# Kernel optimization log

Measured on AMD Instinct MI355X. Metric: run time of the kernel, lower is better.

The kernel has to match this reference:

```python
import jax, jax.numpy as jnp
import numpy as np

N_NODES = 50000
N_EDGES = 1000000
F = 256          # feature_size
NC = 300         # n_content_dims
ED = 64          # embedding_dim = 2**int(log2(F/4))
L = 3            # n_layers


def setup_inputs() -> dict:
    key = jax.random.key(0)
    ks = jax.random.split(key, 20)
    s = 0.05  # weight init scale
    return {
        'node_ids': jnp.arange(N_NODES, dtype=jnp.int32),
        'content': jax.random.normal(ks[0], (N_NODES, NC), jnp.float32),
        'src': jax.random.randint(ks[1], (N_EDGES,), 0, N_NODES, jnp.int32),
        'dst': jax.random.randint(ks[2], (N_EDGES,), 0, N_NODES, jnp.int32),
        'emb': jax.random.normal(ks[3], (N_NODES + 1, ED), jnp.float32) / ED,
        'W_exp': jax.random.normal(ks[4], (F, ED), jnp.float32) * s,
        'b_exp': jnp.zeros((F,), jnp.float32),
        'W_p1': jax.random.normal(ks[5], (NC, NC), jnp.float32) * s,
        'b_p1': jnp.zeros((NC,), jnp.float32),
        'W_p2': jax.random.normal(ks[6], (F, NC), jnp.float32) * s,
        'b_p2': jnp.zeros((F,), jnp.float32),
        'W_conv': jax.random.normal(ks[7], (L, F, 2 * F), jnp.float32) * s,
        'b_conv': jnp.zeros((L, F), jnp.float32),
        'Wo1': jax.random.normal(ks[8], (L - 1, F, F), jnp.float32) * s,
        'bo1': jnp.zeros((L - 1, F), jnp.float32),
        'Wo2': jax.random.normal(ks[9], (L - 1, F, F), jnp.float32) * s,
        'bo2': jnp.zeros((L - 1, F), jnp.float32),
    }


def _lrelu(x):
    return jax.nn.leaky_relu(x, 0.1)


def reference(node_ids, content, src, dst, emb, W_exp, b_exp, W_p1, b_p1,
              W_p2, b_p2, W_conv, b_conv, Wo1, bo1, Wo2, bo2):
    # initial node repr: expansion(node_emb) + proj(content)  (GaussianNoise = identity at eval)
    h = _lrelu(emb[node_ids] @ W_exp.T + b_exp)                 # [N, F]
    c = _lrelu(content @ W_p1.T + b_p1)
    c = _lrelu(c @ W_p2.T + b_p2)
    h = h + c

    ones = jnp.ones((src.shape[0],), h.dtype)
    deg = jax.ops.segment_sum(ones, dst, num_segments=N_NODES)  # in-degree
    w = (deg + 1.0)[:, None]                                    # +1 for self-loop

    for i in range(L):
        # message passing: sum neighbor h (with self-loop), then neighbor mean
        agg = jax.ops.segment_sum(h[src], dst, num_segments=N_NODES) + h  # [N, F]
        h_agg = (agg - h) / jnp.maximum(w - 1.0, 1.0)
        h_concat = jnp.concatenate([h, h_agg], axis=1)          # [N, 2F]
        h_new = h_concat @ W_conv[i].T + b_conv[i]
        if i < L - 1:
            h_new = _lrelu(h_new)
        # L2-normalize rows
        h_new = h_new / jnp.maximum(
            jnp.linalg.norm(h_new, axis=1, keepdims=True), 1e-6)
        if i < L - 1:  # W_out block (non-prediction layers)
            h_new = _lrelu(h_new @ Wo1[i].T + bo1[i])
            h_new = h_new @ Wo2[i].T + bo2[i]
        h = h_new
    return h
```

## Files before the change

kernel.cpp:

```cpp
#include <hip/hip_runtime.h>
#include <stdint.h>

#define NNODES 50000
#define NROWS_PAD 50048
#define NEDGES 1000000
#define FD 256
#define NCPAD 384
#define EDIM 64
#define NSCAN ((NNODES + 255) / 256)

typedef unsigned short u16;
typedef __attribute__((ext_vector_type(8))) short short8;
typedef __attribute__((ext_vector_type(4))) float floatx4;

__device__ __forceinline__ float bf2f(u16 x) {
    union { unsigned u; float f; } c; c.u = ((unsigned)x) << 16; return c.f;
}
__device__ __forceinline__ u16 f2bf(float f) {
    union { float f; unsigned u; } c; c.f = f;
    unsigned u = c.u;
    return (u16)((u + 0x7fffu + ((u >> 16) & 1u)) >> 16);
}
__device__ __forceinline__ void gload16(const u16* g, u16* l) {
    __builtin_amdgcn_global_load_lds(
        (const __attribute__((address_space(1))) void*)g,
        (__attribute__((address_space(3))) void*)l, 16, 0, 0);
}

__global__ void detect_kernel(const u16* p, int* flag) {
    __shared__ int smax;
    if (threadIdx.x == 0) smax = 0;
    __syncthreads();
    int m = 0;
    for (int i = threadIdx.x; i < 8192; i += 256) {
        int e = (p[i] >> 7) & 0xFF;
        m = m > e ? m : e;
    }
    atomicMax(&smax, m);
    __syncthreads();
    if (threadIdx.x == 0) *flag = (smax >= 140) ? 1 : 0;
}

#define NB_CONV 1798
#define NB_CNT4 489
#define PREP_GRID (NB_CONV + NB_CNT4)
__global__ __launch_bounds__(512) void prep_kernel(
    u16* arena, const int* flagp,
    const void* wexp, const void* bexp, const void* wp1, const void* bp1,
    const void* wp2, const void* bp2, const void* wconv, const void* bconv,
    const void* wo1, const void* bo1, const void* wo2, const void* bo2,
    const int* dst, int* deg)
{
    const int bid = blockIdx.x;
    if (bid >= NB_CONV) {
        int q4 = (bid - NB_CONV) * 512 + threadIdx.x;
        if (q4 * 4 + 3 < NEDGES) {
            int4 d = *(const int4*)(dst + q4 * 4);
            atomicAdd(&deg[d.x], 1);
            atomicAdd(&deg[d.y], 1);
            atomicAdd(&deg[d.z], 1);
            atomicAdd(&deg[d.w], 1);
        }
        return;
    }
    const int offs[13]  = {0,16384,16640,164096,164480,262784,263040,
                           656256,657024,788096,788608,919680,920192};
    const int rreal[12] = {256,1,300,1,256,1,768,1,512,1,512,1};
    const int creal[12] = {64,256,300,300,300,256,512,768,256,512,256,512};
    const int cpd[12]   = {64,256,384,384,384,256,512,768,256,512,256,512};
    long gid = (long)bid * 512 + threadIdx.x;
    if (gid >= 920192) return;
    const void* srcs[12] = {wexp,bexp,wp1,bp1,wp2,bp2,wconv,bconv,wo1,bo1,wo2,bo2};
    int fl = *flagp;
    int t = 0;
    #pragma unroll
    for (int i = 1; i < 12; ++i) if (gid >= offs[i]) t = i;
    long local = gid - offs[t];
    int rr = (int)(local / cpd[t]);
    int cc = (int)(local % cpd[t]);
    u16 v = 0;
    if (rr < rreal[t] && cc < creal[t]) {
        long si = (long)rr * creal[t] + cc;
        v = fl ? f2bf(((const float*)srcs[t])[si]) : ((const u16*)srcs[t])[si];
    }
    arena[gid] = v;
}

__global__ __launch_bounds__(256) void scan1_kernel(const int* deg, int* bsum) {
    __shared__ int s[256];
    int t = threadIdx.x;
    int i = blockIdx.x * 256 + t;
    s[t] = (i < NNODES) ? deg[i] : 0;
    __syncthreads();
    #pragma unroll
    for (int off = 128; off > 0; off >>= 1) {
        if (t < off) s[t] += s[t + off];
        __syncthreads();
    }
    if (t == 0) bsum[blockIdx.x] = s[0];
}

__global__ __launch_bounds__(256) void scan2_kernel(int* bsum, int* row_start) {
    __shared__ int s[256];
    int t = threadIdx.x;
    int v = (t < NSCAN) ? bsum[t] : 0;
    s[t] = v;
    __syncthreads();
    for (int off = 1; off < 256; off <<= 1) {
        int x = (t >= off) ? s[t - off] : 0;
        __syncthreads();
        s[t] += x;
        __syncthreads();
    }
    if (t < NSCAN) bsum[t] = s[t] - v;
    if (t == 0) row_start[NNODES] = NEDGES;
}

__global__ __launch_bounds__(256) void scan3_kernel(const int* deg, const int* bsum,
        int* row_start, int* cursor, float* inv_w) {
    __shared__ int s[256];
    int t = threadIdx.x;
    int i = blockIdx.x * 256 + t;
    int v = (i < NNODES) ? deg[i] : 0;
    s[t] = v;
    __syncthreads();
    for (int off = 1; off < 256; off <<= 1) {
        int x = (t >= off) ? s[t - off] : 0;
        __syncthreads();
        s[t] += x;
        __syncthreads();
    }
    if (i < NNODES) {
        int base = bsum[blockIdx.x] + s[t] - v;
        row_start[i] = base;
        cursor[i] = base;
        inv_w[i] = 1.0f / (float)(v > 0 ? v : 1);
    }
}

#define IF_GRID (391 * 7)
__global__ __launch_bounds__(512, 4) void initfill_kernel(
    const void* __restrict__ content, const void* __restrict__ emb,
    const int* __restrict__ flagp,
    const u16* __restrict__ Wp1, const u16* __restrict__ bp1,
    const u16* __restrict__ Wp2, const u16* __restrict__ bp2,
    const u16* __restrict__ Wexp, const u16* __restrict__ bexp,
    u16* __restrict__ hbuf,
    const int* __restrict__ src, const int* __restrict__ dst,
    int* __restrict__ cursor, int* __restrict__ esrc)
{
    __shared__ __align__(16) u16 sA[64 * 64];
    __shared__ __align__(16) u16 sB[384 * 32];
    __shared__ __align__(16) u16 T[64 * 384];

    const int g7 = blockIdx.x / 7, r7 = blockIdx.x % 7;
    if (r7 >= 2) {
        int fb = g7 * 5 + (r7 - 2);
        int e = fb * 512 + threadIdx.x;
        if (e < NEDGES) {
            int v = dst[e];
            int pos = atomicAdd(&cursor[v], 1);
            if ((unsigned)pos < (unsigned)NEDGES) esrc[pos] = src[e];
        }
        return;
    }
    const int bm = (g7 * 2 + r7) * 64;
    const int t = threadIdx.x;
    const int wave = t >> 6, lane = t & 63;
    const int quad = lane >> 4, l16 = lane & 15;
    const int wm = wave >> 2, wn = wave & 3;
    const int lrow = lane >> 2, lcol = (lane & 3) * 8;
    const int fl = *flagp;

    {
        int row = t >> 3;
        int c0 = (t & 7) * 8;
        int gm = bm + row;
        u16 o[8];
        if (gm < NNODES) {
            if (fl) {
                const float* ep = (const float*)emb + (size_t)gm * EDIM + c0;
                float4 x = *(const float4*)ep;
                float4 y = *(const float4*)(ep + 4);
                o[0]=f2bf(x.x); o[1]=f2bf(x.y); o[2]=f2bf(x.z); o[3]=f2bf(x.w);
                o[4]=f2bf(y.x); o[5]=f2bf(y.y); o[6]=f2bf(y.z); o[7]=f2bf(y.w);
            } else {
                const u16* ep = (const u16*)emb + (size_t)gm * EDIM + c0;
                ushort4 x = *(const ushort4*)ep;
                ushort4 y = *(const ushort4*)(ep + 4);
                o[0]=x.x; o[1]=x.y; o[2]=x.z; o[3]=x.w;
                o[4]=y.x; o[5]=y.y; o[6]=y.z; o[7]=y.w;
            }
        } else {
            #pragma unroll
            for (int k = 0; k < 8; ++k) o[k] = 0;
        }
        u16* d = &sA[(row * 64 + c0) ^ ((row & 7) << 3)];
        #pragma unroll
        for (int k = 0; k < 8; ++k) d[k] = o[k];
    }
    #pragma unroll
    for (int j = 0; j < 6; ++j) {
        int idx = (j * 512 + t) * 8;
        int row = idx / 384;
        int c0 = idx % 384;
        int gm = bm + row;
        u16 o[8];
        if (gm < NNODES && c0 + 8 <= 300) {
            if (fl) {
                const float* cp = (const float*)content + (size_t)gm * 300 + c0;
                float4 x = *(const float4*)cp;
                float4 y = *(const float4*)(cp + 4);
                o[0]=f2bf(x.x); o[1]=f2bf(x.y); o[2]=f2bf(x.z); o[3]=f2bf(x.w);
                o[4]=f2bf(y.x); o[5]=f2bf(y.y); o[6]=f2bf(y.z); o[7]=f2bf(y.w);
            } else {
                const u16* cp = (const u16*)content + (size_t)gm * 300 + c0;
                ushort4 x = *(const ushort4*)cp;
                ushort4 y = *(const ushort4*)(cp + 4);
                o[0]=x.x; o[1]=x.y; o[2]=x.z; o[3]=x.w;
                o[4]=y.x; o[5]=y.y; o[6]=y.z; o[7]=y.w;
            }
        } else if (gm < NNODES && c0 < 300) {
            #pragma unroll
            for (int k = 0; k < 8; ++k) {
                int c = c0 + k;
                o[k] = (c < 300)
                    ? (fl ? f2bf(((const float*)content)[(size_t)gm * 300 + c])
                          : ((const u16*)content)[(size_t)gm * 300 + c])
                    : (u16)0;
            }
        } else {
            #pragma unroll
            for (int k = 0; k < 8; ++k) o[k] = 0;
        }
        u16* d = &T[(row * 384 + c0) ^ ((row & 7) << 3)];
        #pragma unroll
        for (int k = 0; k < 8; ++k) d[k] = o[k];
    }
    __syncthreads();

    floatx4 a1[2][6];
    #pragma unroll
    for (int i = 0; i < 2; ++i)
        #pragma unroll
        for (int j = 0; j < 6; ++j) a1[i][j] = (floatx4){0.f, 0.f, 0.f, 0.f};
    for (int kt = 0; kt < 384; kt += 32) {
        #pragma unroll
        for (int c = 0; c < 3; ++c) {
            int r0 = wave * 48 + c * 16;
            gload16(Wp1 + (size_t)(r0 + lrow) * NCPAD + kt + lcol, &sB[r0 * 32]);
        }
        __syncthreads();
        short8 af[2];
        #pragma unroll
        for (int mt = 0; mt < 2; ++mt) {
            int row = wm * 32 + mt * 16 + l16;
            af[mt] = *(const short8*)&T[(row * 384 + kt + quad * 8) ^ ((row & 7) << 3)];
        }
        #pragma unroll
        for (int nt = 0; nt < 6; ++nt) {
            short8 bf = *(const short8*)&sB[(wn * 96 + nt * 16 + l16) * 32 + quad * 8];
            a1[0][nt] = __builtin_amdgcn_mfma_f32_16x16x32_bf16(af[0], bf, a1[0][nt], 0, 0, 0);
            a1[1][nt] = __builtin_amdgcn_mfma_f32_16x16x32_bf16(af[1], bf, a1[1][nt], 0, 0, 0);
        }
        __syncthreads();
    }
    #pragma unroll
    for (int nt = 0; nt < 6; ++nt) {
        int col = wn * 96 + nt * 16 + l16;
        float bv = bf2f(bp1[col]);
        #pragma unroll
        for (int mt = 0; mt < 2; ++mt)
            #pragma unroll
            for (int rr = 0; rr < 4; ++rr) {
                int row = wm * 32 + mt * 16 + quad * 4 + rr;
                float v = a1[mt][nt][rr] + bv;
                v = v > 0.f ? v : 0.1f * v;
                T[(row * NCPAD + col) ^ ((row & 7) << 3)] = f2bf(v);
            }
    }
    __syncthreads();

    floatx4 a2[2][4];
    #pragma unroll
    for (int i = 0; i < 2; ++i)
        #pragma unroll
        for (int j = 0; j < 4; ++j) a2[i][j] = (floatx4){0.f, 0.f, 0.f, 0.f};
    for (int kt = 0; kt < 384; kt += 32) {
        #pragma unroll
        for (int c = 0; c < 2; ++c) {
            int r0 = wave * 32 + c * 16;
            gload16(Wp2 + (size_t)(r0 + lrow) * NCPAD + kt + lcol, &sB[r0 * 32]);
        }
        __syncthreads();
        short8 af[2];
        #pragma unroll
        for (int mt = 0; mt < 2; ++mt) {
            int row = wm * 32 + mt * 16 + l16;
            af[mt] = *(const short8*)&T[(row * NCPAD + kt + quad * 8) ^ ((row & 7) << 3)];
        }
        #pragma unroll
        for (int nt = 0; nt < 4; ++nt) {
            short8 bf = *(const short8*)&sB[(wn * 64 + nt * 16 + l16) * 32 + quad * 8];
            a2[0][nt] = __builtin_amdgcn_mfma_f32_16x16x32_bf16(af[0], bf, a2[0][nt], 0, 0, 0);
            a2[1][nt] = __builtin_amdgcn_mfma_f32_16x16x32_bf16(af[1], bf, a2[1][nt], 0, 0, 0);
        }
        __syncthreads();
    }

    floatx4 aE[2][4];
    #pragma unroll
    for (int i = 0; i < 2; ++i)
        #pragma unroll
        for (int j = 0; j < 4; ++j) aE[i][j] = (floatx4){0.f, 0.f, 0.f, 0.f};
    for (int kt = 0; kt < 64; kt += 32) {
        #pragma unroll
        for (int c = 0; c < 2; ++c) {
            int r0 = wave * 32 + c * 16;
            gload16(Wexp + (size_t)(r0 + lrow) * EDIM + kt + lcol, &sB[r0 * 32]);
        }
        __syncthreads();
        short8 af[2];
        #pragma unroll
        for (int mt = 0; mt < 2; ++mt) {
            int row = wm * 32 + mt * 16 + l16;
            af[mt] = *(const short8*)&sA[(row * 64 + kt + quad * 8) ^ ((row & 7) << 3)];
        }
        #pragma unroll
        for (int nt = 0; nt < 4; ++nt) {
            short8 bf = *(const short8*)&sB[(wn * 64 + nt * 16 + l16) * 32 + quad * 8];
            aE[0][nt] = __builtin_amdgcn_mfma_f32_16x16x32_bf16(af[0], bf, aE[0][nt], 0, 0, 0);
            aE[1][nt] = __builtin_amdgcn_mfma_f32_16x16x32_bf16(af[1], bf, aE[1][nt], 0, 0, 0);
        }
        __syncthreads();
    }

    #pragma unroll
    for (int nt = 0; nt < 4; ++nt) {
        int col = wn * 64 + nt * 16 + l16;
        float bE = bf2f(bexp[col]), b2 = bf2f(bp2[col]);
        #pragma unroll
        for (int mt = 0; mt < 2; ++mt)
            #pragma unroll
            for (int rr = 0; rr < 4; ++rr) {
                int row = wm * 32 + mt * 16 + quad * 4 + rr;
                int gm = bm + row;
                if (gm < NNODES) {
                    float hE = aE[mt][nt][rr] + bE; hE = hE > 0.f ? hE : 0.1f * hE;
                    float c2 = a2[mt][nt][rr] + b2; c2 = c2 > 0.f ? c2 : 0.1f * c2;
                    hbuf[(size_t)gm * FD + col] = f2bf(hE + c2);
                }
            }
    }
}

__global__ __launch_bounds__(512, 4) void layer_kernel(
    const u16* __restrict__ h, const u16* __restrict__ agg,
    const u16* __restrict__ Wc, const u16* __restrict__ bc,
    const u16* __restrict__ W1, const u16* __restrict__ b1,
    const u16* __restrict__ W2, const u16* __restrict__ b2,
    u16* __restrict__ out)
{
    __shared__ __align__(16) u16 sA[2][64 * 32];
    __shared__ __align__(16) u16 sB[2][256 * 32];
    __shared__ __align__(16) u16 T[64 * 256];
    __shared__ float ssq[4][64];

    const int t = threadIdx.x;
    const int wave = t >> 6, lane = t & 63;
    const int quad = lane >> 4, l16 = lane & 15;
    const int wm = wave >> 2, wn = wave & 3;
    const int lrow = lane >> 2, lcol = (lane & 3) * 8;
    const int bm = blockIdx.x * 64;

    floatx4 acc[2][4];
    #pragma unroll
    for (int i = 0; i < 2; ++i)
        #pragma unroll
        for (int j = 0; j < 4; ++j) acc[i][j] = (floatx4){0.f, 0.f, 0.f, 0.f};

    for (int kt = 0; kt < 512; kt += 64) {
        const u16* Ap = (kt < 256) ? h : agg;
        const int kk = kt & 255;
        {
            int hh = wave & 1, r0 = (wave >> 1) * 16;
            gload16(Ap + (size_t)(bm + r0 + lrow) * 256 + kk + hh * 32 + lcol,
                    &sA[hh][r0 * 32]);
        }
        #pragma unroll
        for (int c = 0; c < 4; ++c) {
            int hh = c >> 1, r0 = wave * 32 + (c & 1) * 16;
            gload16(Wc + (size_t)(r0 + lrow) * 512 + kt + hh * 32 + lcol,
                    &sB[hh][r0 * 32]);
        }
        __syncthreads();
        #pragma unroll
        for (int g = 0; g < 2; ++g) {
            short8 af[2], bf[4];
            #pragma unroll
            for (int mt = 0; mt < 2; ++mt)
                af[mt] = *(const short8*)&sA[g][(wm * 32 + mt * 16 + l16) * 32 + quad * 8];
            #pragma unroll
            for (int nt = 0; nt < 4; ++nt)
                bf[nt] = *(const short8*)&sB[g][(wn * 64 + nt * 16 + l16) * 32 + quad * 8];
            #pragma unroll
            for (int mt = 0; mt < 2; ++mt)
                #pragma unroll
                for (int nt = 0; nt < 4; ++nt)
                    acc[mt][nt] = __builtin_amdgcn_mfma_f32_16x16x32_bf16(af[mt], bf[nt], acc[mt][nt], 0, 0, 0);
        }
        __syncthreads();
    }
    {
        float part[2][4];
        #pragma unroll
        for (int mt = 0; mt < 2; ++mt)
            #pragma unroll
            for (int rr = 0; rr < 4; ++rr) part[mt][rr] = 0.f;
        #pragma unroll
        for (int nt = 0; nt < 4; ++nt) {
            float bv = bf2f(bc[wn * 64 + nt * 16 + l16]);
            #pragma unroll
            for (int mt = 0; mt < 2; ++mt)
                #pragma unroll
                for (int rr = 0; rr < 4; ++rr) {
                    float v = acc[mt][nt][rr] + bv;
                    v = v > 0.f ? v : 0.1f * v;
                    part[mt][rr] += v * v;
                }
        }
        #pragma unroll
        for (int off = 1; off < 16; off <<= 1)
            #pragma unroll
            for (int mt = 0; mt < 2; ++mt)
                #pragma unroll
                for (int rr = 0; rr < 4; ++rr)
                    part[mt][rr] += __shfl_xor(part[mt][rr], off);
        if (l16 == 0)
            #pragma unroll
            for (int mt = 0; mt < 2; ++mt)
                #pragma unroll
                for (int rr = 0; rr < 4; ++rr)
                    ssq[wn][wm * 32 + mt * 16 + quad * 4 + rr] = part[mt][rr];
        __syncthreads();
        #pragma unroll
        for (int mt = 0; mt < 2; ++mt)
            #pragma unroll
            for (int rr = 0; rr < 4; ++rr) {
                int row = wm * 32 + mt * 16 + quad * 4 + rr;
                float s = 1.0f / fmaxf(sqrtf(ssq[0][row] + ssq[1][row] +
                                             ssq[2][row] + ssq[3][row]), 1e-6f);
                #pragma unroll
                for (int nt = 0; nt < 4; ++nt) {
                    int col = wn * 64 + nt * 16 + l16;
                    float v = acc[mt][nt][rr] + bf2f(bc[col]);
                    v = v > 0.f ? v : 0.1f * v;
                    T[(row * 256 + col) ^ ((row & 7) << 3)] = f2bf(v * s);
                }
            }
        __syncthreads();
    }

    #pragma unroll
    for (int i = 0; i < 2; ++i)
        #pragma unroll
        for (int j = 0; j < 4; ++j) acc[i][j] = (floatx4){0.f, 0.f, 0.f, 0.f};
    for (int kt = 0; kt < 256; kt += 64) {
        #pragma unroll
        for (int c = 0; c < 4; ++c) {
            int hh = c >> 1, r0 = wave * 32 + (c & 1) * 16;
            gload16(W1 + (size_t)(r0 + lrow) * 256 + kt + hh * 32 + lcol,
                    &sB[hh][r0 * 32]);
        }
        __syncthreads();
        #pragma unroll
        for (int g = 0; g < 2; ++g) {
            short8 af[2], bf[4];
            #pragma unroll
            for (int mt = 0; mt < 2; ++mt) {
                int row = wm * 32 + mt * 16 + l16;
                af[mt] = *(const short8*)&T[(row * 256 + kt + g * 32 + quad * 8) ^ ((row & 7) << 3)];
            }
            #pragma unroll
            for (int nt = 0; nt < 4; ++nt)
                bf[nt] = *(const short8*)&sB[g][(wn * 64 + nt * 16 + l16) * 32 + quad * 8];
            #pragma unroll
            for (int mt = 0; mt < 2; ++mt)
                #pragma unroll
                for (int nt = 0; nt < 4; ++nt)
                    acc[mt][nt] = __builtin_amdgcn_mfma_f32_16x16x32_bf16(af[mt], bf[nt], acc[mt][nt], 0, 0, 0);
        }
        __syncthreads();
    }
    #pragma unroll
    for (int nt = 0; nt < 4; ++nt) {
        int col = wn * 64 + nt * 16 + l16;
        float bv = bf2f(b1[col]);
        #pragma unroll
        for (int mt = 0; mt < 2; ++mt) {
            #pragma unroll
            for (int r = 0; r < 4; ++r) {
                int row = wm * 32 + mt * 16 + quad * 4 + r;
                float v = acc[mt][nt][r] + bv;
                v = v > 0.f ? v : 0.1f * v;
                T[(row * 256 + col) ^ ((row & 7) << 3)] = f2bf(v);
            }
        }
    }
    __syncthreads();

    #pragma unroll
    for (int i = 0; i < 2; ++i)
        #pragma unroll
        for (int j = 0; j < 4; ++j) acc[i][j] = (floatx4){0.f, 0.f, 0.f, 0.f};
    for (int kt = 0; kt < 256; kt += 64) {
        #pragma unroll
        for (int c = 0; c < 4; ++c) {
            int hh = c >> 1, r0 = wave * 32 + (c & 1) * 16;
            gload16(W2 + (size_t)(r0 + lrow) * 256 + kt + hh * 32 + lcol,
                    &sB[hh][r0 * 32]);
        }
        __syncthreads();
        #pragma unroll
        for (int g = 0; g < 2; ++g) {
            short8 af[2], bf[4];
            #pragma unroll
            for (int mt = 0; mt < 2; ++mt) {
                int row = wm * 32 + mt * 16 + l16;
                af[mt] = *(const short8*)&T[(row * 256 + kt + g * 32 + quad * 8) ^ ((row & 7) << 3)];
            }
            #pragma unroll
            for (int nt = 0; nt < 4; ++nt)
                bf[nt] = *(const short8*)&sB[g][(wn * 64 + nt * 16 + l16) * 32 + quad * 8];
            #pragma unroll
            for (int mt = 0; mt < 2; ++mt)
                #pragma unroll
                for (int nt = 0; nt < 4; ++nt)
                    acc[mt][nt] = __builtin_amdgcn_mfma_f32_16x16x32_bf16(af[mt], bf[nt], acc[mt][nt], 0, 0, 0);
        }
        __syncthreads();
    }
    #pragma unroll
    for (int nt = 0; nt < 4; ++nt) {
        int col = wn * 64 + nt * 16 + l16;
        float bv = bf2f(b2[col]);
        #pragma unroll
        for (int mt = 0; mt < 2; ++mt) {
            #pragma unroll
            for (int r = 0; r < 4; ++r) {
                int row = wm * 32 + mt * 16 + quad * 4 + r;
                int gm = bm + row;
                if (gm < NNODES) {
                    float v = acc[mt][nt][r] + bv;
                    out[(size_t)gm * 256 + col] = f2bf(v);
                }
            }
        }
    }
}

__global__ __launch_bounds__(512, 4) void final_kernel(
    const u16* __restrict__ h, const u16* __restrict__ agg,
    const u16* __restrict__ Wc, const u16* __restrict__ bc,
    float* __restrict__ out)
{
    __shared__ __align__(16) u16 sA[2][64 * 32];
    __shared__ __align__(16) u16 sB[2][256 * 32];
    __shared__ float ssq[4][64];

    const int t = threadIdx.x;
    const int wave = t >> 6, lane = t & 63;
    const int quad = lane >> 4, l16 = lane & 15;
    const int wm = wave >> 2, wn = wave & 3;
    const int lrow = lane >> 2, lcol = (lane & 3) * 8;
    const int bm = blockIdx.x * 64;

    floatx4 acc[2][4];
    #pragma unroll
    for (int i = 0; i < 2; ++i)
        #pragma unroll
        for (int j = 0; j < 4; ++j) acc[i][j] = (floatx4){0.f, 0.f, 0.f, 0.f};

    for (int kt = 0; kt < 512; kt += 64) {
        const u16* Ap = (kt < 256) ? h : agg;
        const int kk = kt & 255;
        {
            int hh = wave & 1, r0 = (wave >> 1) * 16;
            gload16(Ap + (size_t)(bm + r0 + lrow) * 256 + kk + hh * 32 + lcol,
                    &sA[hh][r0 * 32]);
        }
        #pragma unroll
        for (int c = 0; c < 4; ++c) {
            int hh = c >> 1, r0 = wave * 32 + (c & 1) * 16;
            gload16(Wc + (size_t)(r0 + lrow) * 512 + kt + hh * 32 + lcol,
                    &sB[hh][r0 * 32]);
        }
        __syncthreads();
        #pragma unroll
        for (int g = 0; g < 2; ++g) {
            short8 af[2], bf[4];
            #pragma unroll
            for (int mt = 0; mt < 2; ++mt)
                af[mt] = *(const short8*)&sA[g][(wm * 32 + mt * 16 + l16) * 32 + quad * 8];
            #pragma unroll
            for (int nt = 0; nt < 4; ++nt)
                bf[nt] = *(const short8*)&sB[g][(wn * 64 + nt * 16 + l16) * 32 + quad * 8];
            #pragma unroll
            for (int mt = 0; mt < 2; ++mt)
                #pragma unroll
                for (int nt = 0; nt < 4; ++nt)
                    acc[mt][nt] = __builtin_amdgcn_mfma_f32_16x16x32_bf16(af[mt], bf[nt], acc[mt][nt], 0, 0, 0);
        }
        __syncthreads();
    }
    float part[2][4];
    #pragma unroll
    for (int mt = 0; mt < 2; ++mt)
        #pragma unroll
        for (int rr = 0; rr < 4; ++rr) part[mt][rr] = 0.f;
    #pragma unroll
    for (int nt = 0; nt < 4; ++nt) {
        float bv = bf2f(bc[wn * 64 + nt * 16 + l16]);
        #pragma unroll
        for (int mt = 0; mt < 2; ++mt)
            #pragma unroll
            for (int rr = 0; rr < 4; ++rr) {
                float v = acc[mt][nt][rr] + bv;
                part[mt][rr] += v * v;
            }
    }
    #pragma unroll
    for (int off = 1; off < 16; off <<= 1)
        #pragma unroll
        for (int mt = 0; mt < 2; ++mt)
            #pragma unroll
            for (int rr = 0; rr < 4; ++rr)
                part[mt][rr] += __shfl_xor(part[mt][rr], off);
    if (l16 == 0)
        #pragma unroll
        for (int mt = 0; mt < 2; ++mt)
            #pragma unroll
            for (int rr = 0; rr < 4; ++rr)
                ssq[wn][wm * 32 + mt * 16 + quad * 4 + rr] = part[mt][rr];
    __syncthreads();
    #pragma unroll
    for (int mt = 0; mt < 2; ++mt)
        #pragma unroll
        for (int rr = 0; rr < 4; ++rr) {
            int row = wm * 32 + mt * 16 + quad * 4 + rr;
            int gm = bm + row;
            float s = 1.0f / fmaxf(sqrtf(ssq[0][row] + ssq[1][row] +
                                         ssq[2][row] + ssq[3][row]), 1e-6f);
            if (gm < NNODES) {
                #pragma unroll
                for (int nt = 0; nt < 4; ++nt) {
                    int col = wn * 64 + nt * 16 + l16;
                    out[(size_t)gm * 256 + col] = (acc[mt][nt][rr] + bf2f(bc[col])) * s;
                }
            }
        }
}

__global__ __launch_bounds__(256) void agg_kernel(
    const u16* h, const int* row_start, const int* esrc,
    const float* inv_w, u16* out)
{
    int gid = blockIdx.x * blockDim.x + threadIdx.x;
    int wid = gid >> 6;
    int lane = gid & 63;
    if (wid >= NNODES) return;
    int e0 = row_start[wid], e1 = row_start[wid + 1];
    e0 = max(0, min(e0, NEDGES));
    e1 = max(e0, min(e1, NEDGES));
    float a0 = 0.f, a1 = 0.f, a2 = 0.f, a3 = 0.f;
    int e = e0;
    for (; e + 4 <= e1; e += 4) {
        int u0 = esrc[e + 0]; if ((unsigned)u0 >= (unsigned)NNODES) u0 = 0;
        int u1 = esrc[e + 1]; if ((unsigned)u1 >= (unsigned)NNODES) u1 = 0;
        int u2 = esrc[e + 2]; if ((unsigned)u2 >= (unsigned)NNODES) u2 = 0;
        int u3 = esrc[e + 3]; if ((unsigned)u3 >= (unsigned)NNODES) u3 = 0;
        ushort4 t0 = *(const ushort4*)(h + (size_t)u0 * FD + lane * 4);
        ushort4 t1 = *(const ushort4*)(h + (size_t)u1 * FD + lane * 4);
        ushort4 t2 = *(const ushort4*)(h + (size_t)u2 * FD + lane * 4);
        ushort4 t3 = *(const ushort4*)(h + (size_t)u3 * FD + lane * 4);
        a0 += bf2f(t0.x) + bf2f(t1.x) + bf2f(t2.x) + bf2f(t3.x);
        a1 += bf2f(t0.y) + bf2f(t1.y) + bf2f(t2.y) + bf2f(t3.y);
        a2 += bf2f(t0.z) + bf2f(t1.z) + bf2f(t2.z) + bf2f(t3.z);
        a3 += bf2f(t0.w) + bf2f(t1.w) + bf2f(t2.w) + bf2f(t3.w);
    }
    for (; e < e1; ++e) {
        int u = esrc[e];
        if ((unsigned)u >= (unsigned)NNODES) u = 0;
        ushort4 tv = *(const ushort4*)(h + (size_t)u * FD + lane * 4);
        a0 += bf2f(tv.x); a1 += bf2f(tv.y); a2 += bf2f(tv.z); a3 += bf2f(tv.w);
    }
    float s = inv_w[wid];
    ushort4 ov;
    ov.x = f2bf(a0 * s); ov.y = f2bf(a1 * s); ov.z = f2bf(a2 * s); ov.w = f2bf(a3 * s);
    *(ushort4*)(out + (size_t)wid * FD + lane * 4) = ov;
}

extern "C" void kernel_launch(void* const* d_in, const int* in_sizes, int n_in,
                              void* d_out, int out_size, void* d_ws, size_t ws_size,
                              hipStream_t stream) {
    const void* content = d_in[1];
    const int* src      = (const int*)d_in[2];
    const int* dst      = (const int*)d_in[3];
    const void* emb     = d_in[4];

    char* ws = (char*)d_ws;
    u16* arena = (u16*)(ws);
    u16* hbuf  = (u16*)(ws + 1840640);
    u16* buf2  = (u16*)(ws + 27465216);
    int*   deg    = (int*)(ws + 78714368);
    int*   rs     = (int*)(ws + 78914560);
    int*   cursor = (int*)(ws + 79114752);
    float* inv_w  = (float*)(ws + 79314944);
    int*   esrc   = (int*)(ws + 79515136);
    int*   bsum   = (int*)(ws + 83515648);
    int*   flag   = (int*)(ws + 83516672);

    u16* aWexp  = arena;            u16* aBexp  = arena + 16384;
    u16* aWp1   = arena + 16640;    u16* aBp1   = arena + 164096;
    u16* aWp2   = arena + 164480;   u16* aBp2   = arena + 262784;
    u16* aWconv = arena + 263040;   u16* aBconv = arena + 656256;
    u16* aWo1   = arena + 657024;   u16* aBo1   = arena + 788096;
    u16* aWo2   = arena + 788608;   u16* aBo2   = arena + 919680;

    const int MB64 = NROWS_PAD / 64;

    detect_kernel<<<1, 256, 0, stream>>>((const u16*)content, flag);
    hipMemsetAsync(deg, 0, (size_t)NNODES * 4, stream);
    prep_kernel<<<PREP_GRID, 512, 0, stream>>>(arena, flag,
        d_in[5], d_in[6], d_in[7], d_in[8], d_in[9], d_in[10], d_in[11],
        d_in[12], d_in[13], d_in[14], d_in[15], d_in[16], dst, deg);

    scan1_kernel<<<NSCAN, 256, 0, stream>>>(deg, bsum);
    scan2_kernel<<<1, 256, 0, stream>>>(bsum, rs);
    scan3_kernel<<<NSCAN, 256, 0, stream>>>(deg, bsum, rs, cursor, inv_w);

    initfill_kernel<<<IF_GRID, 512, 0, stream>>>(content, emb, flag,
        aWp1, aBp1, aWp2, aBp2, aWexp, aBexp, hbuf, src, dst, cursor, esrc);

    for (int i = 0; i < 3; ++i) {
        agg_kernel<<<(NNODES * 64) / 256, 256, 0, stream>>>(hbuf, rs, esrc, inv_w, buf2);
        if (i < 2) {
            layer_kernel<<<dim3(MB64), dim3(512), 0, stream>>>(
                hbuf, buf2,
                aWconv + (size_t)i * FD * 2 * FD, aBconv + (size_t)i * FD,
                aWo1 + (size_t)i * FD * FD, aBo1 + (size_t)i * FD,
                aWo2 + (size_t)i * FD * FD, aBo2 + (size_t)i * FD,
                hbuf);
        } else {
            final_kernel<<<dim3(MB64), dim3(512), 0, stream>>>(
                hbuf, buf2,
                aWconv + (size_t)i * FD * 2 * FD, aBconv + (size_t)i * FD,
                (float*)d_out);
        }
    }
}
```

Before: 655.5 us.

## Vectorize edge fill, rebalance init grid, and unroll neighbor aggregation by eight

The CSR fill inside the init kernel now handles four edges per thread using int4 loads of src and dst. The grid interleaving changes from 2 GEMM blocks plus 5 fill blocks per group to 8 plus 5, so the fill work uses fewer blocks. LDS stores of staged tiles are widened to ushort4, and the aggregation kernel unrolls the gather loop to eight edges with a scalar node id via readfirstlane to expose more loads in flight. More registers per thread may lower occupancy, and the CSR order now depends on a different atomic schedule.

```diff
diff --git a/kernel.cpp b/kernel.cpp
--- a/kernel.cpp
+++ b/kernel.cpp
@@ -53,9 +53,9 @@
 {
     const int bid = blockIdx.x;
     if (bid >= NB_CONV) {
-        int q4 = (bid - NB_CONV) * 512 + threadIdx.x;
-        if (q4 * 4 + 3 < NEDGES) {
-            int4 d = *(const int4*)(dst + q4 * 4);
+        int base = ((bid - NB_CONV) * 512 + threadIdx.x) * 4;
+        if (base < NEDGES) {
+            int4 d = *(const int4*)(dst + base);
             atomicAdd(&deg[d.x], 1);
             atomicAdd(&deg[d.y], 1);
             atomicAdd(&deg[d.z], 1);
@@ -138,7 +138,7 @@
     }
 }
 
-#define IF_GRID (391 * 7)
+#define IF_GRID (98 * 13)
 __global__ __launch_bounds__(512, 4) void initfill_kernel(
     const void* __restrict__ content, const void* __restrict__ emb,
     const int* __restrict__ flagp,
@@ -153,18 +153,28 @@
     __shared__ __align__(16) u16 sB[384 * 32];
     __shared__ __align__(16) u16 T[64 * 384];
 
-    const int g7 = blockIdx.x / 7, r7 = blockIdx.x % 7;
-    if (r7 >= 2) {
-        int fb = g7 * 5 + (r7 - 2);
-        int e = fb * 512 + threadIdx.x;
-        if (e < NEDGES) {
-            int v = dst[e];
-            int pos = atomicAdd(&cursor[v], 1);
-            if ((unsigned)pos < (unsigned)NEDGES) esrc[pos] = src[e];
+    const int g13 = blockIdx.x / 13, r13 = blockIdx.x % 13;
+    if (r13 >= 8) {
+        int fb = g13 * 5 + (r13 - 8);
+        if (fb >= NB_CNT4) return;
+        int base = (fb * 512 + threadIdx.x) * 4;
+        if (base < NEDGES) {
+            int4 s4 = *(const int4*)(src + base);
+            int4 d4 = *(const int4*)(dst + base);
+            int p0 = atomicAdd(&cursor[d4.x], 1);
+            int p1 = atomicAdd(&cursor[d4.y], 1);
+            int p2 = atomicAdd(&cursor[d4.z], 1);
+            int p3 = atomicAdd(&cursor[d4.w], 1);
+            if ((unsigned)p0 < (unsigned)NEDGES) esrc[p0] = s4.x;
+            if ((unsigned)p1 < (unsigned)NEDGES) esrc[p1] = s4.y;
+            if ((unsigned)p2 < (unsigned)NEDGES) esrc[p2] = s4.z;
+            if ((unsigned)p3 < (unsigned)NEDGES) esrc[p3] = s4.w;
         }
         return;
     }
-    const int bm = (g7 * 2 + r7) * 64;
+    const int iid = g13 * 8 + r13;
+    if (iid >= 782) return;
+    const int bm = iid * 64;
     const int t = threadIdx.x;
     const int wave = t >> 6, lane = t & 63;
     const int quad = lane >> 4, l16 = lane & 15;
@@ -196,8 +206,8 @@
             for (int k = 0; k < 8; ++k) o[k] = 0;
         }
         u16* d = &sA[(row * 64 + c0) ^ ((row & 7) << 3)];
-        #pragma unroll
-        for (int k = 0; k < 8; ++k) d[k] = o[k];
+        *(ushort4*)d = (ushort4){o[0], o[1], o[2], o[3]};
+        *(ushort4*)(d + 4) = (ushort4){o[4], o[5], o[6], o[7]};
     }
     #pragma unroll
     for (int j = 0; j < 6; ++j) {
@@ -234,8 +244,8 @@
             for (int k = 0; k < 8; ++k) o[k] = 0;
         }
         u16* d = &T[(row * 384 + c0) ^ ((row & 7) << 3)];
-        #pragma unroll
-        for (int k = 0; k < 8; ++k) d[k] = o[k];
+        *(ushort4*)d = (ushort4){o[0], o[1], o[2], o[3]};
+        *(ushort4*)(d + 4) = (ushort4){o[4], o[5], o[6], o[7]};
     }
     __syncthreads();
 
@@ -666,27 +676,40 @@
     const float* inv_w, u16* out)
 {
     int gid = blockIdx.x * blockDim.x + threadIdx.x;
-    int wid = gid >> 6;
-    int lane = gid & 63;
+    int wid = __builtin_amdgcn_readfirstlane(gid >> 6);
+    int lane = threadIdx.x & 63;
     if (wid >= NNODES) return;
     int e0 = row_start[wid], e1 = row_start[wid + 1];
     e0 = max(0, min(e0, NEDGES));
     e1 = max(e0, min(e1, NEDGES));
     float a0 = 0.f, a1 = 0.f, a2 = 0.f, a3 = 0.f;
     int e = e0;
-    for (; e + 4 <= e1; e += 4) {
+    for (; e + 8 <= e1; e += 8) {
+        int u[8];
+        #pragma unroll
+        for (int k = 0; k < 8; ++k) {
+            u[k] = esrc[e + k];
+            if ((unsigned)u[k] >= (unsigned)NNODES) u[k] = 0;
+        }
+        ushort4 tv[8];
+        #pragma unroll
+        for (int k = 0; k < 8; ++k)
+            tv[k] = *(const ushort4*)(h + (size_t)u[k] * FD + lane * 4);
+        #pragma unroll
+        for (int k = 0; k < 8; ++k) {
+            a0 += bf2f(tv[k].x); a1 += bf2f(tv[k].y);
+            a2 += bf2f(tv[k].z); a3 += bf2f(tv[k].w);
+        }
+    }
+    for (; e + 2 <= e1; e += 2) {
         int u0 = esrc[e + 0]; if ((unsigned)u0 >= (unsigned)NNODES) u0 = 0;
         int u1 = esrc[e + 1]; if ((unsigned)u1 >= (unsigned)NNODES) u1 = 0;
-        int u2 = esrc[e + 2]; if ((unsigned)u2 >= (unsigned)NNODES) u2 = 0;
-        int u3 = esrc[e + 3]; if ((unsigned)u3 >= (unsigned)NNODES) u3 = 0;
         ushort4 t0 = *(const ushort4*)(h + (size_t)u0 * FD + lane * 4);
         ushort4 t1 = *(const ushort4*)(h + (size_t)u1 * FD + lane * 4);
-        ushort4 t2 = *(const ushort4*)(h + (size_t)u2 * FD + lane * 4);
-        ushort4 t3 = *(const ushort4*)(h + (size_t)u3 * FD + lane * 4);
-        a0 += bf2f(t0.x) + bf2f(t1.x) + bf2f(t2.x) + bf2f(t3.x);
-        a1 += bf2f(t0.y) + bf2f(t1.y) + bf2f(t2.y) + bf2f(t3.y);
-        a2 += bf2f(t0.z) + bf2f(t1.z) + bf2f(t2.z) + bf2f(t3.z);
-        a3 += bf2f(t0.w) + bf2f(t1.w) + bf2f(t2.w) + bf2f(t3.w);
+        a0 += bf2f(t0.x) + bf2f(t1.x);
+        a1 += bf2f(t0.y) + bf2f(t1.y);
+        a2 += bf2f(t0.z) + bf2f(t1.z);
+        a3 += bf2f(t0.w) + bf2f(t1.w);
     }
     for (; e < e1; ++e) {
         int u = esrc[e];
```

Result: no change. 644.8 us (-1.6%).
